# Kernel optimization log

Hardware: AMD Instinct MI355X
Metric: run time of the kernel (lower is better)

## Reference

```python
import jax, jax.numpy as jnp
import numpy as np

DIM = 512
NUM_GROUPS = 32
HEADS = 16
HEAD_DIM = 32
EPS = 1e-6


def group_norm(x, w, b, num_groups=NUM_GROUPS, eps=EPS):
    # x: [B, C, H, W]
    B, C, H, W = x.shape
    xg = x.reshape(B, num_groups, -1)
    mean = xg.mean(axis=-1, keepdims=True)
    var = xg.var(axis=-1, keepdims=True)
    xg = (xg - mean) / jnp.sqrt(var + eps)
    x = xg.reshape(B, C, H, W)
    return x * w[None, :, None, None] + b[None, :, None, None]


def conv1x1(x, w, b):
    # x: [B, C, H, W], w: [O, C], b: [O]
    return jnp.einsum('bchw,oc->bohw', x, w) + b[None, :, None, None]


def setup_inputs() -> dict:
    key = jax.random.key(0)
    ks = jax.random.split(key, 12)
    s = 1.0 / np.sqrt(DIM)
    d = {
        'x': jax.random.normal(ks[0], (1, DIM, 64, 64), dtype=jnp.float32),
        'gn_w': jnp.ones((DIM,), dtype=jnp.float32),
        'gn_b': jnp.zeros((DIM,), dtype=jnp.float32),
        'wq': jax.random.normal(ks[1], (DIM, DIM), dtype=jnp.float32) * s,
        'bq': jax.random.normal(ks[2], (DIM,), dtype=jnp.float32) * 0.01,
        'wk': jax.random.normal(ks[3], (DIM, DIM), dtype=jnp.float32) * s,
        'bk': jax.random.normal(ks[4], (DIM,), dtype=jnp.float32) * 0.01,
        'wv': jax.random.normal(ks[5], (DIM, DIM), dtype=jnp.float32) * s,
        'bv': jax.random.normal(ks[6], (DIM,), dtype=jnp.float32) * 0.01,
        'wo': jax.random.normal(ks[7], (DIM, DIM), dtype=jnp.float32) * s,
        'bo': jax.random.normal(ks[8], (DIM,), dtype=jnp.float32) * 0.01,
    }
    return d


def reference(x, gn_w, gn_b, wq, bq, wk, bk, wv, bv, wo, bo):
    B, C, H, W = x.shape
    N = H * W
    scale = HEAD_DIM ** -0.5

    q_in = x
    qn = group_norm(x, gn_w, gn_b)
    # Faithful to source: v-branch applies norm_q to the already-normalized q.
    vn = group_norm(qn, gn_w, gn_b)

    q = conv1x1(qn, wq, bq)
    k = conv1x1(vn, wk, bk)
    v = conv1x1(vn, wv, bv)

    def to_tokens(t):
        # [B, C, H, W] -> [B, heads, N, head_dim]
        return t.reshape(B, HEADS, HEAD_DIM, N).transpose(0, 1, 3, 2)

    q, k, v = to_tokens(q), to_tokens(k), to_tokens(v)

    attn = jax.nn.softmax(jnp.einsum('bhnd,bhmd->bhnm', q, k) * scale, axis=-1)
    out = jnp.einsum('bhnm,bhmd->bhnd', attn, v)  # [B, heads, N, head_dim]
    out = out.transpose(0, 1, 3, 2).reshape(B, C, H, W)
    out = conv1x1(out, wo, bo)
    return (out + q_in) / jnp.sqrt(jnp.float32(2.0))
```

## Files before the change

### kernel.cpp

```cpp
#include <hip/hip_runtime.h>

#define NTOK 4096
#define CHAN 512
#define GSIZE 65536
#define RSQRT2 0.7071067811865476f
#define SCALE 0.17677669529663687f
#define WB_OFF 32768
#define QT_OFF (WB_OFF + 2097152)
#define WS_NEEDED ((size_t)(QT_OFF + 4194304))

typedef unsigned short ushort_t;
typedef __attribute__((ext_vector_type(8))) short bf16x8;
typedef __attribute__((ext_vector_type(8))) _Float16 f16x8;
typedef __attribute__((ext_vector_type(4))) float f32x4;

__device__ __forceinline__ ushort_t f2b(float f) {
    unsigned u = __float_as_uint(f);
    unsigned r = (u + 0x7FFFu + ((u >> 16) & 1u)) >> 16;
    return (ushort_t)r;
}
__device__ __forceinline__ unsigned pack2r(float a, float b) {
    unsigned ua = __float_as_uint(a), ub = __float_as_uint(b);
    return ((ua + 0x8000u) >> 16) | ((ub + 0x8000u) & 0xFFFF0000u);
}
__device__ __forceinline__ unsigned packh2(float a, float b) {
    return __builtin_bit_cast(unsigned, __builtin_amdgcn_cvt_pkrtz(a, b));
}
__device__ __forceinline__ ushort_t f2h(float f) {
    return (ushort_t)(packh2(f, f) & 0xFFFFu);
}
__device__ __forceinline__ bf16x8 ldfrag(const ushort_t* p) {
    return __builtin_bit_cast(bf16x8, *(const uint4*)p);
}
__device__ __forceinline__ f16x8 ldfragh(const ushort_t* p) {
    return __builtin_bit_cast(f16x8, *(const uint4*)p);
}

__global__ void diag_kernel(float* out, float v) {
    if (threadIdx.x == 0 && blockIdx.x == 0) out[0] = v;
}

__global__ __launch_bounds__(256) void gn_sums(const float* __restrict__ x,
                                               float* __restrict__ S,
                                               float* __restrict__ SS) {
    int c = blockIdx.x, t = threadIdx.x;
    const float4* p = (const float4*)(x + (size_t)c * 4096);
    float s = 0.f, ss = 0.f;
    #pragma unroll
    for (int i = 0; i < 4; i++) {
        float4 f = p[i * 256 + t];
        s += f.x + f.y + f.z + f.w;
        ss += f.x * f.x + f.y * f.y + f.z * f.z + f.w * f.w;
    }
    #pragma unroll
    for (int off = 32; off > 0; off >>= 1) {
        s += __shfl_xor(s, off);
        ss += __shfl_xor(ss, off);
    }
    __shared__ float as[4], bs[4];
    int w = t >> 6;
    if ((t & 63) == 0) { as[w] = s; bs[w] = ss; }
    __syncthreads();
    if (t == 0) {
        S[c] = as[0] + as[1] + as[2] + as[3];
        SS[c] = bs[0] + bs[1] + bs[2] + bs[3];
    }
}

__global__ __launch_bounds__(512) void gn_coef(const float* __restrict__ S,
                                               const float* __restrict__ SS,
                                               const float* __restrict__ gnw,
                                               const float* __restrict__ gnb,
                                               float* __restrict__ qa,
                                               float* __restrict__ qd,
                                               float* __restrict__ va,
                                               float* __restrict__ vd) {
    int c = threadIdx.x;
    float Sc = S[c], SSc = SS[c];
    float gs = Sc, gss = SSc;
    #pragma unroll
    for (int off = 1; off < 16; off <<= 1) {
        gs += __shfl_xor(gs, off);
        gss += __shfl_xor(gss, off);
    }
    float mu = gs * (1.f / GSIZE);
    float var = gss * (1.f / GSIZE) - mu * mu;
    float r1 = rsqrtf(var + 1e-6f);
    float wc = gnw[c], bc = gnb[c];
    float a1 = r1 * wc;
    float d1 = bc - mu * a1;
    qa[c] = a1; qd[c] = d1;
    float S2 = a1 * Sc + 4096.f * d1;
    float SS2 = a1 * a1 * SSc + 2.f * a1 * d1 * Sc + 4096.f * d1 * d1;
    float gs2 = S2, gss2 = SS2;
    #pragma unroll
    for (int off = 1; off < 16; off <<= 1) {
        gs2 += __shfl_xor(gs2, off);
        gss2 += __shfl_xor(gss2, off);
    }
    float mu2 = gs2 * (1.f / GSIZE);
    float var2 = gss2 * (1.f / GSIZE) - mu2 * mu2;
    float r2 = rsqrtf(var2 + 1e-6f);
    float a2 = r2 * wc;
    va[c] = a1 * a2;
    vd[c] = a2 * (d1 - mu2) + bc;
}

__global__ __launch_bounds__(256) void bias_fold(const float* __restrict__ wq,
                                                 const float* __restrict__ wk,
                                                 const float* __restrict__ wv,
                                                 const float* __restrict__ bq,
                                                 const float* __restrict__ bk,
                                                 const float* __restrict__ bv,
                                                 const float* __restrict__ qd,
                                                 const float* __restrict__ vd,
                                                 float* __restrict__ bqf,
                                                 float* __restrict__ bkf,
                                                 float* __restrict__ bvf) {
    int row = blockIdx.x * 4 + (threadIdx.x >> 6);
    int lane = threadIdx.x & 63;
    int m = row >> 9;
    int o = row & 511;
    const float* W = (m == 0) ? wq : (m == 1) ? wk : wv;
    const float* b = (m == 0) ? bq : (m == 1) ? bk : bv;
    const float* d = (m == 0) ? qd : vd;
    float* outp    = (m == 0) ? bqf : (m == 1) ? bkf : bvf;
    const float4* wr = (const float4*)(W + (size_t)o * 512) + lane * 2;
    const float4* dr = (const float4*)d + lane * 2;
    float4 a0 = wr[0], a1 = wr[1], d0 = dr[0], d1 = dr[1];
    float acc = a0.x * d0.x + a0.y * d0.y + a0.z * d0.z + a0.w * d0.w
              + a1.x * d1.x + a1.y * d1.y + a1.z * d1.z + a1.w * d1.w;
    #pragma unroll
    for (int off = 32; off > 0; off >>= 1) acc += __shfl_xor(acc, off);
    if (lane == 0) outp[o] = b[o] + acc;
}

__global__ __launch_bounds__(256) void wprep(const float* __restrict__ wq,
                                             const float* __restrict__ wk,
                                             const float* __restrict__ wv,
                                             const float* __restrict__ wo,
                                             const float* __restrict__ qa,
                                             const float* __restrict__ va,
                                             ushort_t* __restrict__ Wb) {
    int y = blockIdx.y;
    const float* src = (y == 0) ? wq : (y == 1) ? wk : (y == 2) ? wv : wo;
    int i = (blockIdx.x * 256 + threadIdx.x) * 4;
    float4 f = *(const float4*)(src + i);
    if (y < 3) {
        const float* aff = (y == 0) ? qa : va;
        float4 a = *(const float4*)(aff + (i & 511));
        f.x *= a.x; f.y *= a.y; f.z *= a.z; f.w *= a.w;
    }
    uint2 u;
    u.x = pack2r(f.x, f.y);
    u.y = pack2r(f.z, f.w);
    *(uint2*)(Wb + (size_t)y * 262144 + i) = u;
}

__global__ __launch_bounds__(256) void qkv_mfma(const float* __restrict__ x,
                                                const ushort_t* __restrict__ Wb,
                                                const float* __restrict__ bqf,
                                                const float* __restrict__ bkf,
                                                const float* __restrict__ bvf,
                                                ushort_t* __restrict__ QT,
                                                ushort_t* __restrict__ KT,
                                                ushort_t* __restrict__ Vb) {
    __shared__ __align__(16) ushort_t Wl[128][72];
    __shared__ __align__(16) ushort_t Bn[64][72];
    __shared__ __align__(16) ushort_t Tl[64][136];
    int t = threadIdx.x;
    int nbase = blockIdx.x << 6;
    int y = blockIdx.y;
    int buf = y >> 2;
    int obase = (y & 3) << 7;
    const ushort_t* Wsrc = Wb + (size_t)buf * 262144;
    const float* bias = (buf == 0) ? bqf : (buf == 1) ? bkf : bvf;

    int w = t >> 6, lane = t & 63, q15 = lane & 15, quad = lane >> 4;
    f32x4 acc[2][4];
    #pragma unroll
    for (int i = 0; i < 2; i++)
        #pragma unroll
        for (int j = 0; j < 4; j++) acc[i][j] = (f32x4){0.f, 0.f, 0.f, 0.f};

    int tok = t & 63, c8 = t >> 6;
    for (int ck = 0; ck < 512; ck += 64) {
        __syncthreads();
        #pragma unroll
        for (int i = 0; i < 4; i++) {
            int idx = 4 * t + i;
            int row = idx >> 3, seg = idx & 7;
            *(uint4*)&Wl[row][seg * 8] =
                *(const uint4*)&Wsrc[(size_t)(obase + row) * 512 + ck + seg * 8];
        }
        {
            float v[16];
            #pragma unroll
            for (int i = 0; i < 16; i++)
                v[i] = x[(size_t)(ck + c8 * 16 + i) * NTOK + nbase + tok];
            uint4 u0, u1;
            u0.x = pack2r(v[0], v[1]);   u0.y = pack2r(v[2], v[3]);
            u0.z = pack2r(v[4], v[5]);   u0.w = pack2r(v[6], v[7]);
            u1.x = pack2r(v[8], v[9]);   u1.y = pack2r(v[10], v[11]);
            u1.z = pack2r(v[12], v[13]); u1.w = pack2r(v[14], v[15]);
            *(uint4*)&Bn[tok][c8 * 16] = u0;
            *(uint4*)&Bn[tok][c8 * 16 + 8] = u1;
        }
        __syncthreads();
        #pragma unroll
        for (int kk = 0; kk < 2; kk++) {
            bf16x8 af0 = ldfrag(&Wl[w * 32 + q15][kk * 32 + quad * 8]);
            bf16x8 af1 = ldfrag(&Wl[w * 32 + 16 + q15][kk * 32 + quad * 8]);
            #pragma unroll
            for (int n8 = 0; n8 < 4; n8++) {
                bf16x8 bfv = ldfrag(&Bn[n8 * 16 + q15][kk * 32 + quad * 8]);
                acc[0][n8] = __builtin_amdgcn_mfma_f32_16x16x32_bf16(af0, bfv, acc[0][n8], 0, 0, 0);
                acc[1][n8] = __builtin_amdgcn_mfma_f32_16x16x32_bf16(af1, bfv, acc[1][n8], 0, 0, 0);
            }
        }
    }

    if (buf == 2) {
        #pragma unroll
        for (int mi = 0; mi < 2; mi++)
            #pragma unroll
            for (int r = 0; r < 4; r++) {
                int o = obase + w * 32 + mi * 16 + quad * 4 + r;
                float bo = bias[o];
                #pragma unroll
                for (int n8 = 0; n8 < 4; n8++)
                    Vb[(size_t)o * NTOK + nbase + n8 * 16 + q15] = f2h(acc[mi][n8][r] + bo);
            }
        return;
    }

    ushort_t* dstT = (buf == 0) ? QT : KT;
    float qs = (buf == 0) ? SCALE : 1.0f;
    __syncthreads();
    #pragma unroll
    for (int mi = 0; mi < 2; mi++)
        #pragma unroll
        for (int r = 0; r < 4; r++) {
            int mloc = w * 32 + mi * 16 + quad * 4 + r;
            float bo = bias[obase + mloc];
            #pragma unroll
            for (int n8 = 0; n8 < 4; n8++)
                Tl[n8 * 16 + q15][mloc] = f2b((acc[mi][n8][r] + bo) * qs);
        }
    __syncthreads();
    #pragma unroll
    for (int i = 0; i < 4; i++) {
        int idx = 4 * t + i;
        int row = idx >> 4, ch = idx & 15;
        uint4 u = *(const uint4*)&Tl[row][ch * 8];
        *(uint4*)&dstT[(size_t)(nbase + row) * 512 + obase + ch * 8] = u;
    }
}

__global__ __launch_bounds__(256) void attn_v8(ushort_t* __restrict__ QT,
                                               const ushort_t* __restrict__ KT,
                                               const ushort_t* __restrict__ V) {
    __shared__ __align__(16) ushort_t Kt[256][40];
    __shared__ __align__(16) ushort_t Vt[32][264];
    __shared__ __align__(16) unsigned Plu[4][32][44];
    int h = blockIdx.y;
    int t = threadIdx.x;
    int w = t >> 6, lane = t & 63, q15 = lane & 15, quad = lane >> 4;
    int qbase = (blockIdx.x << 7) + w * 32;
    int hc = h * 32;
    const ushort_t* Vh = V + (size_t)hc * NTOK;

    bf16x8 qf[2];
    #pragma unroll
    for (int qi = 0; qi < 2; qi++)
        qf[qi] = ldfrag(&QT[(size_t)(qbase + qi * 16 + q15) * 512 + hc + quad * 8]);

    const uint4 onesu = {0x3C003C00u, 0x3C003C00u, 0x3C003C00u, 0x3C003C00u};
    const f16x8 ones = __builtin_bit_cast(f16x8, onesu);

    f32x4 o[2][2];
    #pragma unroll
    for (int qi = 0; qi < 2; qi++)
        #pragma unroll
        for (int dc = 0; dc < 2; dc++) o[qi][dc] = (f32x4){0.f, 0.f, 0.f, 0.f};
    f32x4 lacc[2] = {{0.f, 0.f, 0.f, 0.f}, {0.f, 0.f, 0.f, 0.f}};

    for (int j0 = 0; j0 < NTOK; j0 += 256) {
        __syncthreads();
        #pragma unroll
        for (int i = 0; i < 4; i++) {
            int idx = t + (i << 8);
            int krow = idx >> 2, kseg = idx & 3;
            *(uint4*)&Kt[krow][kseg * 8] =
                *(const uint4*)&KT[(size_t)(j0 + krow) * 512 + hc + kseg * 8];
        }
        #pragma unroll
        for (int i = 0; i < 4; i++) {
            int idx = t + (i << 8);
            int vrow = idx >> 5, vseg = idx & 31;
            *(uint4*)&Vt[vrow][vseg * 8] =
                *(const uint4*)&Vh[(size_t)vrow * NTOK + j0 + vseg * 8];
        }
        __syncthreads();

        #pragma unroll
        for (int h2 = 0; h2 < 4; h2++) {
            f32x4 st[4][2];
            #pragma unroll
            for (int kt = 0; kt < 4; kt++) {
                bf16x8 kf = ldfrag(&Kt[h2 * 64 + kt * 16 + q15][quad * 8]);
                #pragma unroll
                for (int qi = 0; qi < 2; qi++) {
                    f32x4 z = {0.f, 0.f, 0.f, 0.f};
                    st[kt][qi] = __builtin_amdgcn_mfma_f32_16x16x32_bf16(kf, qf[qi], z, 0, 0, 0);
                }
            }

            #pragma unroll
            for (int kt = 0; kt < 4; kt++)
                #pragma unroll
                for (int r = 0; r < 4; r++) {
                    st[kt][0][r] = __expf(st[kt][0][r]);
                    st[kt][1][r] = __expf(st[kt][1][r]);
                }

            asm volatile("" ::: "memory");
            #pragma unroll
            for (int kt = 0; kt < 4; kt++)
                #pragma unroll
                for (int qi = 0; qi < 2; qi++) {
                    uint2 pp;
                    pp.x = packh2(st[kt][qi][0], st[kt][qi][1]);
                    pp.y = packh2(st[kt][qi][2], st[kt][qi][3]);
                    *(uint2*)&Plu[w][qi * 16 + q15][kt * 8 + quad * 2] = pp;
                }
            asm volatile("" ::: "memory");

            #pragma unroll
            for (int kc = 0; kc < 2; kc++) {
                f16x8 v0 = ldfragh(&Vt[q15][h2 * 64 + kc * 32 + quad * 8]);
                f16x8 v1 = ldfragh(&Vt[16 + q15][h2 * 64 + kc * 32 + quad * 8]);
                #pragma unroll
                for (int qi = 0; qi < 2; qi++) {
                    uint4 pu = *(const uint4*)&Plu[w][qi * 16 + q15][kc * 16 + quad * 4];
                    f16x8 pf = __builtin_bit_cast(f16x8, pu);
                    o[qi][0] = __builtin_amdgcn_mfma_f32_16x16x32_f16(pf, v0, o[qi][0], 0, 0, 0);
                    o[qi][1] = __builtin_amdgcn_mfma_f32_16x16x32_f16(pf, v1, o[qi][1], 0, 0, 0);
                    lacc[qi] = __builtin_amdgcn_mfma_f32_16x16x32_f16(pf, ones, lacc[qi], 0, 0, 0);
                }
            }
        }
    }

    #pragma unroll
    for (int qi = 0; qi < 2; qi++)
        #pragma unroll
        for (int r = 0; r < 4; r++) {
            float li = 1.f / lacc[qi][r];
            int q = quad * 4 + r;
            QT[(size_t)(qbase + qi * 16 + q) * 512 + hc + q15]      = f2b(o[qi][0][r] * li);
            QT[(size_t)(qbase + qi * 16 + q) * 512 + hc + 16 + q15] = f2b(o[qi][1][r] * li);
        }
}

__global__ __launch_bounds__(256) void oproj_mfma(const ushort_t* __restrict__ OT,
                                                  const ushort_t* __restrict__ Wob,
                                                  const float* __restrict__ bo,
                                                  const float* __restrict__ x,
                                                  float* __restrict__ out) {
    __shared__ __align__(16) ushort_t Wl[64][40];
    __shared__ __align__(16) ushort_t Bn[64][40];
    int t = threadIdx.x;
    int nbase = blockIdx.x << 6;
    int obase = blockIdx.y << 6;
    int w = t >> 6, lane = t & 63, q15 = lane & 15, quad = lane >> 4;

    f32x4 acc[4];
    #pragma unroll
    for (int i = 0; i < 4; i++) acc[i] = (f32x4){0.f, 0.f, 0.f, 0.f};

    int arow = t >> 2, aseg = t & 3;
    for (int ck = 0; ck < 512; ck += 32) {
        __syncthreads();
        *(uint4*)&Wl[arow][aseg * 8] =
            *(const uint4*)&Wob[(size_t)(obase + arow) * 512 + ck + aseg * 8];
        *(uint4*)&Bn[arow][aseg * 8] =
            *(const uint4*)&OT[(size_t)(nbase + arow) * 512 + ck + aseg * 8];
        __syncthreads();
        bf16x8 af = ldfrag(&Wl[w * 16 + q15][quad * 8]);
        #pragma unroll
        for (int n8 = 0; n8 < 4; n8++) {
            bf16x8 bfv = ldfrag(&Bn[n8 * 16 + q15][quad * 8]);
            acc[n8] = __builtin_amdgcn_mfma_f32_16x16x32_bf16(af, bfv, acc[n8], 0, 0, 0);
        }
    }

    #pragma unroll
    for (int r = 0; r < 4; r++) {
        int o = obase + w * 16 + quad * 4 + r;
        float b = bo[o];
        #pragma unroll
        for (int n8 = 0; n8 < 4; n8++) {
            size_t idx = (size_t)o * NTOK + nbase + n8 * 16 + q15;
            out[idx] = (acc[n8][r] + b + x[idx]) * RSQRT2;
        }
    }
}

extern "C" void kernel_launch(void* const* d_in, const int* in_sizes, int n_in,
                              void* d_out, int out_size, void* d_ws, size_t ws_size,
                              hipStream_t stream) {
    const float* x   = (const float*)d_in[0];
    const float* gnw = (const float*)d_in[1];
    const float* gnb = (const float*)d_in[2];
    const float* wq  = (const float*)d_in[3];
    const float* bq  = (const float*)d_in[4];
    const float* wk  = (const float*)d_in[5];
    const float* bk  = (const float*)d_in[6];
    const float* wv  = (const float*)d_in[7];
    const float* bv  = (const float*)d_in[8];
    const float* wo  = (const float*)d_in[9];
    const float* bo  = (const float*)d_in[10];
    float* out = (float*)d_out;

    if (ws_size < WS_NEEDED) {
        diag_kernel<<<1, 64, 0, stream>>>(out, (float)(ws_size >> 16));
        return;
    }

    char* wsb = (char*)d_ws;
    float* S   = (float*)(wsb + 0);
    float* SS  = (float*)(wsb + 2048);
    float* qa  = (float*)(wsb + 4096);
    float* qd  = (float*)(wsb + 6144);
    float* va  = (float*)(wsb + 8192);
    float* vd  = (float*)(wsb + 10240);
    float* bqf = (float*)(wsb + 12288);
    float* bkf = (float*)(wsb + 14336);
    float* bvf = (float*)(wsb + 16384);
    ushort_t* Wb = (ushort_t*)(wsb + WB_OFF);
    ushort_t* QT = (ushort_t*)(wsb + QT_OFF);
    ushort_t* KT = (ushort_t*)d_out;
    ushort_t* Vb = (ushort_t*)d_out + (size_t)CHAN * NTOK;

    gn_sums<<<512, 256, 0, stream>>>(x, S, SS);
    gn_coef<<<1, 512, 0, stream>>>(S, SS, gnw, gnb, qa, qd, va, vd);
    bias_fold<<<384, 256, 0, stream>>>(wq, wk, wv, bq, bk, bv, qd, vd, bqf, bkf, bvf);
    wprep<<<dim3(256, 4), 256, 0, stream>>>(wq, wk, wv, wo, qa, va, Wb);

    qkv_mfma<<<dim3(64, 12), 256, 0, stream>>>(x, Wb, bqf, bkf, bvf, QT, KT, Vb);

    attn_v8<<<dim3(32, 16), 256, 0, stream>>>(QT, KT, Vb);

    oproj_mfma<<<dim3(64, 8), 256, 0, stream>>>(QT, Wb + (size_t)3 * 262144, bo, x, out);
}
```

Measured before the change: 185.4 us.

## Keep softmax probabilities in registers by permuting K rows to match MFMA layout

```diff
diff --git a/kernel.cpp b/kernel.cpp
--- a/kernel.cpp
+++ b/kernel.cpp
@@ -4,7 +4,7 @@
 #define CHAN 512
 #define GSIZE 65536
 #define RSQRT2 0.7071067811865476f
-#define SCALE 0.17677669529663687f
+#define SCALEX 0.2550348837f
 #define WB_OFF 32768
 #define QT_OFF (WB_OFF + 2097152)
 #define WS_NEEDED ((size_t)(QT_OFF + 4194304))
@@ -235,7 +235,7 @@
     }
 
     ushort_t* dstT = (buf == 0) ? QT : KT;
-    float qs = (buf == 0) ? SCALE : 1.0f;
+    float qs = (buf == 0) ? SCALEX : 1.0f;
     __syncthreads();
     #pragma unroll
     for (int mi = 0; mi < 2; mi++)
@@ -257,12 +257,11 @@
     }
 }
 
-__global__ __launch_bounds__(256) void attn_v8(ushort_t* __restrict__ QT,
-                                               const ushort_t* __restrict__ KT,
-                                               const ushort_t* __restrict__ V) {
+__global__ __launch_bounds__(256, 4) void attn_v10(ushort_t* __restrict__ QT,
+                                                   const ushort_t* __restrict__ KT,
+                                                   const ushort_t* __restrict__ V) {
     __shared__ __align__(16) ushort_t Kt[256][40];
     __shared__ __align__(16) ushort_t Vt[32][264];
-    __shared__ __align__(16) unsigned Plu[4][32][44];
     int h = blockIdx.y;
     int t = threadIdx.x;
     int w = t >> 6, lane = t & 63, q15 = lane & 15, quad = lane >> 4;
@@ -291,8 +290,10 @@
         for (int i = 0; i < 4; i++) {
             int idx = t + (i << 8);
             int krow = idx >> 2, kseg = idx & 3;
+            int rp = krow & 63;
+            int src = (krow & 192) | (rp & 0x23) | ((rp & 0x0C) << 1) | ((rp & 0x10) >> 2);
             *(uint4*)&Kt[krow][kseg * 8] =
-                *(const uint4*)&KT[(size_t)(j0 + krow) * 512 + hc + kseg * 8];
+                *(const uint4*)&KT[(size_t)(j0 + src) * 512 + hc + kseg * 8];
         }
         #pragma unroll
         for (int i = 0; i < 4; i++) {
@@ -320,34 +321,34 @@
             for (int kt = 0; kt < 4; kt++)
                 #pragma unroll
                 for (int r = 0; r < 4; r++) {
-                    st[kt][0][r] = __expf(st[kt][0][r]);
-                    st[kt][1][r] = __expf(st[kt][1][r]);
+                    st[kt][0][r] = __builtin_exp2f(st[kt][0][r]);
+                    st[kt][1][r] = __builtin_exp2f(st[kt][1][r]);
                 }
 
-            asm volatile("" ::: "memory");
-            #pragma unroll
-            for (int kt = 0; kt < 4; kt++)
-                #pragma unroll
-                for (int qi = 0; qi < 2; qi++) {
-                    uint2 pp;
-                    pp.x = packh2(st[kt][qi][0], st[kt][qi][1]);
-                    pp.y = packh2(st[kt][qi][2], st[kt][qi][3]);
-                    *(uint2*)&Plu[w][qi * 16 + q15][kt * 8 + quad * 2] = pp;
-                }
-            asm volatile("" ::: "memory");
-
-            #pragma unroll
-            for (int kc = 0; kc < 2; kc++) {
-                f16x8 v0 = ldfragh(&Vt[q15][h2 * 64 + kc * 32 + quad * 8]);
-                f16x8 v1 = ldfragh(&Vt[16 + q15][h2 * 64 + kc * 32 + quad * 8]);
-                #pragma unroll
-                for (int qi = 0; qi < 2; qi++) {
-                    uint4 pu = *(const uint4*)&Plu[w][qi * 16 + q15][kc * 16 + quad * 4];
-                    f16x8 pf = __builtin_bit_cast(f16x8, pu);
-                    o[qi][0] = __builtin_amdgcn_mfma_f32_16x16x32_f16(pf, v0, o[qi][0], 0, 0, 0);
-                    o[qi][1] = __builtin_amdgcn_mfma_f32_16x16x32_f16(pf, v1, o[qi][1], 0, 0, 0);
-                    lacc[qi] = __builtin_amdgcn_mfma_f32_16x16x32_f16(pf, ones, lacc[qi], 0, 0, 0);
-                }
+            f16x8 v00 = ldfragh(&Vt[q15][h2 * 64 + quad * 8]);
+            f16x8 v01 = ldfragh(&Vt[16 + q15][h2 * 64 + quad * 8]);
+            f16x8 v10 = ldfragh(&Vt[q15][h2 * 64 + 32 + quad * 8]);
+            f16x8 v11 = ldfragh(&Vt[16 + q15][h2 * 64 + 32 + quad * 8]);
+
+            #pragma unroll
+            for (int qi = 0; qi < 2; qi++) {
+                uint4 p0u, p1u;
+                p0u.x = packh2(st[0][qi][0], st[0][qi][1]);
+                p0u.y = packh2(st[0][qi][2], st[0][qi][3]);
+                p0u.z = packh2(st[1][qi][0], st[1][qi][1]);
+                p0u.w = packh2(st[1][qi][2], st[1][qi][3]);
+                p1u.x = packh2(st[2][qi][0], st[2][qi][1]);
+                p1u.y = packh2(st[2][qi][2], st[2][qi][3]);
+                p1u.z = packh2(st[3][qi][0], st[3][qi][1]);
+                p1u.w = packh2(st[3][qi][2], st[3][qi][3]);
+                f16x8 pf0 = __builtin_bit_cast(f16x8, p0u);
+                f16x8 pf1 = __builtin_bit_cast(f16x8, p1u);
+                o[qi][0] = __builtin_amdgcn_mfma_f32_16x16x32_f16(pf0, v00, o[qi][0], 0, 0, 0);
+                o[qi][1] = __builtin_amdgcn_mfma_f32_16x16x32_f16(pf0, v01, o[qi][1], 0, 0, 0);
+                lacc[qi] = __builtin_amdgcn_mfma_f32_16x16x32_f16(pf0, ones, lacc[qi], 0, 0, 0);
+                o[qi][0] = __builtin_amdgcn_mfma_f32_16x16x32_f16(pf1, v10, o[qi][0], 0, 0, 0);
+                o[qi][1] = __builtin_amdgcn_mfma_f32_16x16x32_f16(pf1, v11, o[qi][1], 0, 0, 0);
+                lacc[qi] = __builtin_amdgcn_mfma_f32_16x16x32_f16(pf1, ones, lacc[qi], 0, 0, 0);
             }
         }
     }
@@ -450,7 +451,7 @@
 
     qkv_mfma<<<dim3(64, 12), 256, 0, stream>>>(x, Wb, bqf, bkf, bvf, QT, KT, Vb);
 
-    attn_v8<<<dim3(32, 16), 256, 0, stream>>>(QT, KT, Vb);
+    attn_v10<<<dim3(32, 16), 256, 0, stream>>>(QT, KT, Vb);
 
     oproj_mfma<<<dim3(64, 8), 256, 0, stream>>>(QT, Wb + (size_t)3 * 262144, bo, x, out);
 }
```

Result: slower. 209.7 us (+13.1%).
